# Performance work log

Measured on AMD Instinct MI355X. Metric: run time of the kernel, lower is better.

Reference implementation:

```python
import jax, jax.numpy as jnp
import numpy as np

N, E, L, F, HID, OUT = 20000, 200000, 5, 4, 128, 3


def _lin(x, w, b):
    # torch Linear convention: w is [out, in]
    return x @ w.T + b


def setup_inputs() -> dict:
    key = jax.random.key(0)
    ks = iter(jax.random.split(key, 40))
    nrm = lambda shape, s=0.05: jax.random.normal(next(ks), shape, dtype=jnp.float32) * s
    inp = {
        'x': jax.random.normal(next(ks), (N, L, F), dtype=jnp.float32),
        'edge_index': jax.random.randint(next(ks), (2, E), 0, N, dtype=jnp.int64),
        'edge_attr': jax.random.normal(next(ks), (E, F), dtype=jnp.float32),
        'batch': jnp.zeros((N,), dtype=jnp.int64),
        'node_type': jax.random.normal(next(ks), (N, 1), dtype=jnp.float32),
        # PastStateEncoder params
        'emb': nrm((L, F), 1.0),
        'conv_w': nrm((HID, 2 * F, 3)),  # Conv1d(8,128,3) OIW
        'conv_b': nrm((HID,)),
        # FusionLayer Linear(129,128)
        'fuse_w': nrm((HID, HID + 1)), 'fuse_b': nrm((HID,)),
        # gnn1 EdgeModel: Linear(2*128+4,128), Linear(128,128)
        'g1e_w1': nrm((HID, 2 * HID + F)), 'g1e_b1': nrm((HID,)),
        'g1e_w2': nrm((HID, HID)), 'g1e_b2': nrm((HID,)),
        # gnn1 NodeModel: Linear(256,128), Linear(128,128)
        'g1n_w1': nrm((HID, 2 * HID)), 'g1n_b1': nrm((HID,)),
        'g1n_w2': nrm((HID, HID)), 'g1n_b2': nrm((HID,)),
        # gnn2 EdgeModel: Linear(2*128+128,128), Linear(128,128)
        'g2e_w1': nrm((HID, 3 * HID)), 'g2e_b1': nrm((HID,)),
        'g2e_w2': nrm((HID, HID)), 'g2e_b2': nrm((HID,)),
        # gnn2 NodeModel
        'g2n_w1': nrm((HID, 2 * HID)), 'g2n_b1': nrm((HID,)),
        'g2n_w2': nrm((HID, HID)), 'g2n_b2': nrm((HID,)),
        # final_mlp: Linear(128,128), BN(128), Linear(128,3)
        'fm_w1': nrm((HID, HID)), 'fm_b1': nrm((HID,)),
        'bn_g': jnp.ones((HID,), dtype=jnp.float32), 'bn_b': jnp.zeros((HID,), dtype=jnp.float32),
        'fm_w2': nrm((OUT, HID)), 'fm_b2': nrm((OUT,)),
    }
    return inp


def _encoder(x, emb, conv_w, conv_b):
    # x: [N, L, F]; append learned positional embedding -> [N, L, 2F]
    n = x.shape[0]
    xe = jnp.concatenate([x, jnp.broadcast_to(emb[None], (n, L, F))], axis=-1)
    xc = xe.transpose(0, 2, 1)  # [N, 2F, L]
    y = jax.lax.conv_general_dilated(
        xc, conv_w, window_strides=(1,), padding=[(1, 1)],
        dimension_numbers=('NCW', 'OIW', 'NCW'))
    y = y + conv_b[None, :, None]
    return y.mean(axis=-1)  # [N, HID]


def _edge_mlp(src, dst, ea, w1, b1, w2, b2):
    h = jax.nn.relu(_lin(jnp.concatenate([src, dst, ea], axis=1), w1, b1))
    return _lin(h, w2, b2)


def _node_mlp(x_row, ea, w1, b1, w2, b2):
    h = jax.nn.relu(_lin(jnp.concatenate([x_row, ea], axis=1), w1, b1))
    return _lin(h, w2, b2)


def reference(x, edge_index, edge_attr, batch, node_type,
              emb, conv_w, conv_b, fuse_w, fuse_b,
              g1e_w1, g1e_b1, g1e_w2, g1e_b2, g1n_w1, g1n_b1, g1n_w2, g1n_b2,
              g2e_w1, g2e_b1, g2e_w2, g2e_b2, g2n_w1, g2n_b1, g2n_w2, g2n_b2,
              fm_w1, fm_b1, bn_g, bn_b, fm_w2, fm_b2):
    row, col = edge_index[0], edge_index[1]
    h = _encoder(x, emb, conv_w, conv_b)                     # [N,128]
    h = _lin(jnp.concatenate([h, node_type], axis=-1), fuse_w, fuse_b)  # [N,128]
    # gnn1 (MetaLayer: edge model then node model; node model here is per-edge)
    ea = _edge_mlp(h[row], h[col], edge_attr, g1e_w1, g1e_b1, g1e_w2, g1e_b2)  # [E,128]
    h = _node_mlp(h[row], ea, g1n_w1, g1n_b1, g1n_w2, g1n_b2)                  # [E,128]
    # gnn2 (h now lives on edges; indices < N <= E remain valid, matching torch)
    ea = _edge_mlp(h[row], h[col], ea, g2e_w1, g2e_b1, g2e_w2, g2e_b2)
    h = _node_mlp(h[row], ea, g2n_w1, g2n_b1, g2n_w2, g2n_b2)
    # final head on edge_attr: Linear -> BatchNorm1d (training stats) -> ReLU -> Linear
    z = _lin(ea, fm_w1, fm_b1)
    mu = z.mean(axis=0)
    var = z.var(axis=0)  # biased, matches torch BN normalization
    z = (z - mu) * jax.lax.rsqrt(var + 1e-5) * bn_g + bn_b
    z = jax.nn.relu(z)
    return _lin(z, fm_w2, fm_b2)  # [E,3]
```

## Files before the change

### kernel.cpp

```cpp
#include <hip/hip_runtime.h>

#define N_NODES 20000
#define N_EDGES 200000
#define HID 128
#define STR 136
#define NBLK 3125
#define NREP 64

typedef unsigned short u16;
using bf16x8 = __attribute__((ext_vector_type(8))) __bf16;
using f32x4  = __attribute__((ext_vector_type(4))) float;

__device__ __forceinline__ u16 f2bf(float f) {
  union { float f; unsigned u; } v; v.f = f;
  unsigned u = v.u;
  return (u16)((u + 0x7FFFu + ((u >> 16) & 1u)) >> 16);
}
__device__ __forceinline__ float bf2f(unsigned s) {
  union { unsigned u; float f; } v; v.u = s << 16;
  return v.f;
}
__device__ __forceinline__ bf16x8 ld8(const u16* p) { return *(const bf16x8*)p; }

__device__ __forceinline__ void zero_acc(f32x4 acc[4][2]) {
#pragma unroll
  for (int i = 0; i < 4; ++i) {
    acc[i][0] = (f32x4){0.f, 0.f, 0.f, 0.f};
    acc[i][1] = (f32x4){0.f, 0.f, 0.f, 0.f};
  }
}

template <int KSTEPS, typename AF>
__device__ __forceinline__ void wgemm(const u16* __restrict__ PW, AF afrag,
                                      f32x4 acc[4][2], int lane, int wave) {
  const u16* pb = PW + (wave * 2 * 64 + lane) * 8;
  bf16x8 b0[2], b1[2];
  b0[0] = ld8(pb);
  b1[0] = ld8(pb + 512);
#pragma unroll
  for (int ks = 0; ks < KSTEPS; ++ks) {
    const int cur = ks & 1, nxt = cur ^ 1;
    if (ks + 1 < KSTEPS) {
      b0[nxt] = ld8(pb + (ks + 1) * 4096);
      b1[nxt] = ld8(pb + (ks + 1) * 4096 + 512);
    }
#pragma unroll
    for (int mt = 0; mt < 4; ++mt) {
      bf16x8 a = afrag(ks, mt);
      acc[mt][0] = __builtin_amdgcn_mfma_f32_16x16x32_bf16(a, b0[cur], acc[mt][0], 0, 0, 0);
      acc[mt][1] = __builtin_amdgcn_mfma_f32_16x16x32_bf16(a, b1[cur], acc[mt][1], 0, 0, 0);
    }
  }
}

template <bool RELU>
__device__ __forceinline__ void epi_store(u16* buf, const f32x4 acc[4][2],
                                          const float* __restrict__ bias,
                                          int lane, int wave) {
  const int c = lane & 15, q = lane >> 4;
  const float bb0 = bias[wave * 32 + c], bb1 = bias[wave * 32 + 16 + c];
#pragma unroll
  for (int mt = 0; mt < 4; ++mt)
#pragma unroll
    for (int nt = 0; nt < 2; ++nt) {
      const float bb = nt ? bb1 : bb0;
      const int col = wave * 32 + nt * 16 + c;
#pragma unroll
      for (int r = 0; r < 4; ++r) {
        float v = acc[mt][nt][r] + bb;
        if (RELU) v = fmaxf(v, 0.f);
        buf[(mt * 16 + q * 4 + r) * STR + col] = f2bf(v);
      }
    }
}

__device__ __forceinline__ void flush_buf(const u16* buf, u16* __restrict__ gout,
                                          int e0, int tid) {
#pragma unroll
  for (int it = 0; it < 4; ++it) {
    int cid = tid + it * 256, e = cid >> 4, p = cid & 15;
    uint4 v = *(const uint4*)(buf + e * STR + p * 8);
    *(uint4*)(gout + (size_t)(e0 + e) * HID + p * 8) = v;
  }
}

__device__ __forceinline__ void stage_gather(const int* __restrict__ rowI,
                                             const int* __restrict__ colI,
                                             const u16* __restrict__ htab,
                                             u16* B0, u16* B1,
                                             int e0, int lane, int wave) {
  const int r = lane >> 4, p = lane & 15;
#pragma unroll
  for (int it = 0; it < 8; ++it) {
    int j = wave * 32 + it * 4 + r;
    int e = j & 63;
    int id = (j < 64) ? rowI[e0 + e] : colI[e0 + e];
    uint4 v = *(const uint4*)(htab + (size_t)id * HID + p * 8);
    *(uint4*)(((j < 64) ? B0 : B1) + e * STR + p * 8) = v;
  }
}

__global__ __launch_bounds__(128) void k_prep1(
    const float* __restrict__ emb, const float* __restrict__ conv_w,
    const float* __restrict__ conv_b, const float* __restrict__ fuse_w,
    const float* __restrict__ fuse_b,
    const float* __restrict__ fm_w1, const float* __restrict__ g2e_b2,
    const float* __restrict__ fm_b1, const float* __restrict__ w6,
    float* __restrict__ Mt, float* __restrict__ C0, float* __restrict__ Wnt,
    float* __restrict__ b67, float* __restrict__ W67) {
  __shared__ float red[22][129];
  __shared__ float w7s[128];
  const int o = blockIdx.x;
  const int j = threadIdx.x;
  float A[21];
  {
    float b0 = conv_b[j];
#pragma unroll
    for (int p = 0; p < 5; ++p) {
#pragma unroll
      for (int i = 0; i < 8; ++i) {
        float s = 0.f;
#pragma unroll
        for (int k = 0; k < 3; ++k) {
          int t = p + 1 - k;
          if (t >= 0 && t < 5) s += conv_w[(j * 8 + i) * 3 + k];
        }
        s *= 0.2f;
        if (i < 4) A[p * 4 + i] = s;
        else b0 += emb[p * 4 + (i - 4)] * s;
      }
    }
    A[20] = b0;
  }
  float w = fuse_w[o * 129 + j];
  float w7 = fm_w1[o * 128 + j];
  w7s[j] = w7;
#pragma unroll
  for (int qq = 0; qq < 21; ++qq) red[qq][j] = w * A[qq];
  red[21][j] = w7 * g2e_b2[j];
  __syncthreads();
  if (j < 22) {
    float s = 0.f;
    for (int t = 0; t < 128; ++t) s += red[j][t];
    if (j < 20)      Mt[j * 128 + o] = s;
    else if (j == 20) C0[o] = s + fuse_b[o];
    else              b67[o] = s + fm_b1[o];
  }
  if (j == 0) Wnt[o] = fuse_w[o * 129 + 128];
  float s = 0.f;
  for (int t = 0; t < 128; ++t) s += w7s[t] * w6[t * 128 + j];
  W67[o * 128 + j] = s;
}

struct PackArgs {
  const float* src[6];
  u16* dst[6];
  int Kin[6];
  int ksCum[7];
};

__global__ __launch_bounds__(256) void k_prep2(
    PackArgs pa, const float* __restrict__ x, const float* __restrict__ node_type,
    const float* __restrict__ Mt, const float* __restrict__ C0,
    const float* __restrict__ Wnt, u16* __restrict__ h2) {
  if (blockIdx.x < 41) {
    int bk = blockIdx.x;
    int mi = 0;
    while (bk >= pa.ksCum[mi + 1]) ++mi;
    int ks = bk - pa.ksCum[mi];
    const float* W = pa.src[mi];
    u16* D = pa.dst[mi] + ks * 4096;
    int Kin = pa.Kin[mi];
#pragma unroll
    for (int t = 0; t < 16; ++t) {
      int el = t * 256 + (int)threadIdx.x;
      int j = el & 7, ln = (el >> 3) & 63, ntile = el >> 9;
      int k = ks * 32 + ((ln >> 4) << 3) + j;
      int n = ntile * 16 + (ln & 15);
      float v = (k < Kin) ? W[n * Kin + k] : 0.0f;
      D[el] = f2bf(v);
    }
    return;
  }
  __shared__ float xs[16][20], nts[16], mts[20 * 128];
  const int tid = threadIdx.x;
  const int n0 = ((int)blockIdx.x - 41) * 16;
  for (int i = tid; i < 320; i += 256) xs[i / 20][i % 20] = x[n0 * 20 + i];
  if (tid < 16) nts[tid] = node_type[n0 + tid];
  for (int i = tid; i < 2560; i += 256) mts[i] = Mt[i];
  __syncthreads();
  const int nl = tid >> 4;
  const int c0 = (tid & 15) * 8;
  float nt = nts[nl];
  union { u16 s[8]; uint4 u; } o;
#pragma unroll
  for (int i = 0; i < 8; ++i) {
    int ch = c0 + i;
    float acc = C0[ch] + Wnt[ch] * nt;
#pragma unroll
    for (int qq = 0; qq < 20; ++qq) acc += xs[nl][qq] * mts[qq * 128 + ch];
    o.s[i] = f2bf(acc);
  }
  *(uint4*)(h2 + (size_t)(n0 + nl) * HID + c0) = o.u;
}

__global__ __launch_bounds__(256, 4) void k_gnn1(
    const int* __restrict__ eidx, const float* __restrict__ eattr,
    const u16* __restrict__ h2, const u16* __restrict__ pW1, const u16* __restrict__ pW2,
    const u16* __restrict__ pW3, const u16* __restrict__ pW4, const float* __restrict__ b1,
    const float* __restrict__ b2, const float* __restrict__ b3, const float* __restrict__ b4,
    u16* __restrict__ ea1, u16* __restrict__ h3) {
  __shared__ __align__(16) u16 B0[64 * STR], B1[64 * STR];
  const int tid = threadIdx.x, lane = tid & 63, wave = tid >> 6;
  const int e0 = blockIdx.x * 64;
  const int m = lane & 15, q = lane >> 4;
  const int aoff = m * STR + q * 8;
  const int* rowI = eidx;
  const int* colI = eidx + N_EDGES;

  stage_gather(rowI, colI, h2, B0, B1, e0, lane, wave);

  bf16x8 ef[4];
#pragma unroll
  for (int mt = 0; mt < 4; ++mt) {
    union { u16 s[8]; uint4 u; bf16x8 v; } t;
    t.u = make_uint4(0u, 0u, 0u, 0u);
    if (q == 0) {
      float4 a = *(const float4*)(eattr + (size_t)(e0 + mt * 16 + m) * 4);
      t.s[0] = f2bf(a.x); t.s[1] = f2bf(a.y); t.s[2] = f2bf(a.z); t.s[3] = f2bf(a.w);
    }
    ef[mt] = t.v;
  }
  __syncthreads();

  f32x4 acc[4][2];
  zero_acc(acc);
  wgemm<9>(pW1, [&](int ks, int mt) -> bf16x8 {
    if (ks < 4) return ld8(B0 + aoff + mt * 16 * STR + ks * 32);
    if (ks < 8) return ld8(B1 + aoff + mt * 16 * STR + (ks - 4) * 32);
    return ef[mt];
  }, acc, lane, wave);
  __syncthreads();
  epi_store<true>(B1, acc, b1, lane, wave);
  __syncthreads();

  zero_acc(acc);
  wgemm<4>(pW2, [&](int ks, int mt) -> bf16x8 {
    return ld8(B1 + aoff + mt * 16 * STR + ks * 32);
  }, acc, lane, wave);
  epi_store<false>(B0, acc, b2, lane, wave);
  __syncthreads();
  flush_buf(B0, ea1, e0, tid);

  if (e0 < N_NODES) {
#pragma unroll
    for (int it = 0; it < 4; ++it) {
      int e = wave * 16 + it * 4 + q;
      int id = rowI[e0 + e];
      uint4 v = *(const uint4*)(h2 + (size_t)id * HID + m * 8);
      *(uint4*)(B1 + e * STR + m * 8) = v;
    }
    __syncthreads();

    zero_acc(acc);
    wgemm<8>(pW3, [&](int ks, int mt) -> bf16x8 {
      if (ks < 4) return ld8(B1 + aoff + mt * 16 * STR + ks * 32);
      return ld8(B0 + aoff + mt * 16 * STR + (ks - 4) * 32);
    }, acc, lane, wave);
    __syncthreads();
    epi_store<true>(B1, acc, b3, lane, wave);
    __syncthreads();

    zero_acc(acc);
    wgemm<4>(pW4, [&](int ks, int mt) -> bf16x8 {
      return ld8(B1 + aoff + mt * 16 * STR + ks * 32);
    }, acc, lane, wave);
    epi_store<false>(B0, acc, b4, lane, wave);
    __syncthreads();
    flush_buf(B0, h3, e0, tid);
  }
}

__global__ __launch_bounds__(256, 4) void k_gnn2(
    const int* __restrict__ eidx, const u16* __restrict__ h3, u16* ea1z,
    const u16* __restrict__ pW5, const u16* __restrict__ pW67,
    const float* __restrict__ b5, const float* __restrict__ b67,
    float* __restrict__ bnrep) {
  __shared__ __align__(16) u16 B0[64 * STR], B1[64 * STR];
  const int tid = threadIdx.x, lane = tid & 63, wave = tid >> 6;
  const int e0 = blockIdx.x * 64;
  const int m = lane & 15, q = lane >> 4;
  const int aoff = m * STR + q * 8;
  const int* rowI = eidx;
  const int* colI = eidx + N_EDGES;

  stage_gather(rowI, colI, h3, B0, B1, e0, lane, wave);
  __syncthreads();

  f32x4 acc[4][2];
  zero_acc(acc);
  wgemm<8>(pW5, [&](int ks, int mt) -> bf16x8 {
    if (ks < 4) return ld8(B0 + aoff + mt * 16 * STR + ks * 32);
    return ld8(B1 + aoff + mt * 16 * STR + (ks - 4) * 32);
  }, acc, lane, wave);
  __syncthreads();

#pragma unroll
  for (int it = 0; it < 4; ++it) {
    int cid = tid + it * 256, e = cid >> 4, p = cid & 15;
    uint4 v = *(const uint4*)(ea1z + (size_t)(e0 + e) * HID + p * 8);
    *(uint4*)(B0 + e * STR + p * 8) = v;
  }
  __syncthreads();

  wgemm<4>(pW5 + 8 * 4096, [&](int ks, int mt) -> bf16x8 {
    return ld8(B0 + aoff + mt * 16 * STR + ks * 32);
  }, acc, lane, wave);
  epi_store<true>(B1, acc, b5, lane, wave);
  __syncthreads();

  zero_acc(acc);
  wgemm<4>(pW67, [&](int ks, int mt) -> bf16x8 {
    return ld8(B1 + aoff + mt * 16 * STR + ks * 32);
  }, acc, lane, wave);

  {
    const int c = lane & 15;
    const float bb0 = b67[wave * 32 + c], bb1 = b67[wave * 32 + 16 + c];
    float s0 = 0.f, q0 = 0.f, s1 = 0.f, q1 = 0.f;
#pragma unroll
    for (int mt = 0; mt < 4; ++mt)
#pragma unroll
      for (int r = 0; r < 4; ++r) {
        float v0 = acc[mt][0][r] + bb0;
        float v1 = acc[mt][1][r] + bb1;
        s0 += v0; q0 += v0 * v0;
        s1 += v1; q1 += v1 * v1;
        int row = mt * 16 + q * 4 + r;
        B0[row * STR + wave * 32 + c] = f2bf(v0);
        B0[row * STR + wave * 32 + 16 + c] = f2bf(v1);
      }
    s0 += __shfl_xor(s0, 16); s0 += __shfl_xor(s0, 32);
    q0 += __shfl_xor(q0, 16); q0 += __shfl_xor(q0, 32);
    s1 += __shfl_xor(s1, 16); s1 += __shfl_xor(s1, 32);
    q1 += __shfl_xor(q1, 16); q1 += __shfl_xor(q1, 32);
    if (lane < 16) {
      float* slot = bnrep + ((int)blockIdx.x & (NREP - 1)) * 256;
      atomicAdd(&slot[wave * 32 + lane], s0);
      atomicAdd(&slot[wave * 32 + 16 + lane], s1);
      atomicAdd(&slot[128 + wave * 32 + lane], q0);
      atomicAdd(&slot[128 + wave * 32 + 16 + lane], q1);
    }
  }
  __syncthreads();
  flush_buf(B0, ea1z, e0, tid);
}

__global__ __launch_bounds__(256) void k_head(const u16* __restrict__ z,
                                              const float* __restrict__ bnrep,
                                              const float* __restrict__ bn_g,
                                              const float* __restrict__ bn_b,
                                              const float* __restrict__ w2,
                                              const float* __restrict__ b2,
                                              float* __restrict__ out) {
  __shared__ float sh_s[128], sh_h[128], sh_w0[128], sh_w1[128], sh_w2[128];
  const int tid = threadIdx.x;
  {
    float s = 0.f;
    for (int r = 0; r < NREP; ++r) s += bnrep[r * 256 + tid];
    __shared__ float acc2[256];
    acc2[tid] = s;
    __syncthreads();
    if (tid < 128) {
      const float inv = 1.0f / (float)N_EDGES;
      float mu = acc2[tid] * inv;
      float var = acc2[128 + tid] * inv - mu * mu;
      float sc = bn_g[tid] * rsqrtf(var + 1e-5f);
      sh_s[tid] = sc;
      sh_h[tid] = bn_b[tid] - mu * sc;
      sh_w0[tid] = w2[tid];
      sh_w1[tid] = w2[128 + tid];
      sh_w2[tid] = w2[256 + tid];
    }
    __syncthreads();
  }
  const int lane = tid & 63, wave = tid >> 6;
  const int g = lane >> 4;
  const int p = lane & 15;
  const int c0 = p * 8;
  const float bb0 = b2[0], bb1 = b2[1], bb2 = b2[2];
#pragma unroll 4
  for (int it = 0; it < 16; ++it) {
    int e = (int)blockIdx.x * 256 + wave * 64 + it * 4 + g;
    if (e >= N_EDGES) break;
    uint4 v = *(const uint4*)(z + (size_t)e * HID + c0);
    unsigned wv[4] = {v.x, v.y, v.z, v.w};
    float a0 = 0.f, a1 = 0.f, a2 = 0.f;
#pragma unroll
    for (int k = 0; k < 4; ++k) {
      int ch = c0 + k * 2;
      float lo = bf2f(wv[k] & 0xffffu), hi = bf2f(wv[k] >> 16);
      float r0 = fmaxf(fmaf(lo, sh_s[ch], sh_h[ch]), 0.f);
      float r1 = fmaxf(fmaf(hi, sh_s[ch + 1], sh_h[ch + 1]), 0.f);
      a0 += r0 * sh_w0[ch] + r1 * sh_w0[ch + 1];
      a1 += r0 * sh_w1[ch] + r1 * sh_w1[ch + 1];
      a2 += r0 * sh_w2[ch] + r1 * sh_w2[ch + 1];
    }
#pragma unroll
    for (int off = 1; off < 16; off <<= 1) {
      a0 += __shfl_xor(a0, off);
      a1 += __shfl_xor(a1, off);
      a2 += __shfl_xor(a2, off);
    }
    if (p < 3) out[e * 3 + p] = (p == 0) ? a0 + bb0 : (p == 1) ? a1 + bb1 : a2 + bb2;
  }
}

extern "C" void kernel_launch(void* const* d_in, const int* in_sizes, int n_in,
                              void* d_out, int out_size, void* d_ws, size_t ws_size,
                              hipStream_t stream) {
  const float* x         = (const float*)d_in[0];
  const int* eidx        = (const int*)d_in[1];
  const float* eattr     = (const float*)d_in[2];
  const float* node_type = (const float*)d_in[4];
  const float* emb       = (const float*)d_in[5];
  const float* conv_w    = (const float*)d_in[6];
  const float* conv_b    = (const float*)d_in[7];
  const float* fuse_w    = (const float*)d_in[8];
  const float* fuse_b    = (const float*)d_in[9];
  const float* g1e_w1    = (const float*)d_in[10];
  const float* g1e_b1    = (const float*)d_in[11];
  const float* g1e_w2    = (const float*)d_in[12];
  const float* g1e_b2    = (const float*)d_in[13];
  const float* g1n_w1    = (const float*)d_in[14];
  const float* g1n_b1    = (const float*)d_in[15];
  const float* g1n_w2    = (const float*)d_in[16];
  const float* g1n_b2    = (const float*)d_in[17];
  const float* g2e_w1    = (const float*)d_in[18];
  const float* g2e_b1    = (const float*)d_in[19];
  const float* g2e_w2    = (const float*)d_in[20];
  const float* g2e_b2    = (const float*)d_in[21];
  const float* fm_w1     = (const float*)d_in[26];
  const float* fm_b1     = (const float*)d_in[27];
  const float* bn_g      = (const float*)d_in[28];
  const float* bn_b      = (const float*)d_in[29];
  const float* fm_w2     = (const float*)d_in[30];
  const float* fm_b2     = (const float*)d_in[31];
  float* out = (float*)d_out;

  char* ws = (char*)d_ws;
  size_t off = 0;
  auto take = [&](size_t bytes) {
    void* p = ws + off;
    off = (off + bytes + 255) & ~(size_t)255;
    return p;
  };
  u16* h2   = (u16*)take((size_t)N_NODES * HID * 2);
  u16* h3   = (u16*)take((size_t)20032 * HID * 2);
  u16* ea1z = (u16*)take((size_t)N_EDGES * HID * 2);
  float* Mt    = (float*)take(20 * 128 * 4);
  float* C0    = (float*)take(128 * 4);
  float* Wnt   = (float*)take(128 * 4);
  float* b67   = (float*)take(128 * 4);
  float* W67f  = (float*)take(128 * 128 * 4);
  float* bnrep = (float*)take((size_t)NREP * 256 * 4);
  u16* pW1  = (u16*)take(9 * 4096 * 2);
  u16* pW2  = (u16*)take(4 * 4096 * 2);
  u16* pW3  = (u16*)take(8 * 4096 * 2);
  u16* pW4  = (u16*)take(4 * 4096 * 2);
  u16* pW5  = (u16*)take(12 * 4096 * 2);
  u16* pW67 = (u16*)take(4 * 4096 * 2);

  hipMemsetAsync(bnrep, 0, (size_t)NREP * 256 * 4, stream);
  k_prep1<<<128, 128, 0, stream>>>(emb, conv_w, conv_b, fuse_w, fuse_b,
                                   fm_w1, g2e_b2, fm_b1, g2e_w2,
                                   Mt, C0, Wnt, b67, W67f);

  PackArgs pa;
  const float* srcs[6] = {g1e_w1, g1e_w2, g1n_w1, g1n_w2, g2e_w1, W67f};
  u16* dsts[6] = {pW1, pW2, pW3, pW4, pW5, pW67};
  int kins[6] = {260, 128, 256, 128, 384, 128};
  int kst[6] = {9, 4, 8, 4, 12, 4};
  int cum = 0;
  for (int i = 0; i < 6; ++i) {
    pa.src[i] = srcs[i]; pa.dst[i] = dsts[i]; pa.Kin[i] = kins[i];
    pa.ksCum[i] = cum; cum += kst[i];
  }
  pa.ksCum[6] = cum;

  k_prep2<<<41 + N_NODES / 16, 256, 0, stream>>>(pa, x, node_type, Mt, C0, Wnt, h2);
  k_gnn1<<<NBLK, 256, 0, stream>>>(eidx, eattr, h2, pW1, pW2, pW3, pW4,
                                   g1e_b1, g1e_b2, g1n_b1, g1n_b2, ea1z, h3);
  k_gnn2<<<NBLK, 256, 0, stream>>>(eidx, h3, ea1z, pW5, pW67,
                                   g2e_b1, b67, bnrep);
  k_head<<<(N_EDGES + 255) / 256, 256, 0, stream>>>(ea1z, bnrep, bn_g, bn_b,
                                                    fm_w2, fm_b2, out);
}
```

Baseline: 236.8 us.

## Split GNN edge tiles across eight waves and fold BN-stat zeroing into prep

The two GNN kernels move from 4 waves per 64-edge block, each computing 32 output columns, to 8 waves per block, each computing 16 columns. Per-thread accumulators and B-fragment prefetch are halved, and the gather and flush loops are rebalanced over 512 threads. The aim is more resident waves per CU and lower register pressure so gather latency is better hidden. In exchange each wave does less MFMA work per A-fragment load from LDS, so LDS traffic rises. Separately, the hipMemsetAsync of the BN statistics buffer is replaced by zeroing it inside k_prep1, which drops one launch.

Result: no change. 232.4 us (median of 2 runs) (-1.9%).

```diff
diff --git a/kernel.cpp b/kernel.cpp
--- a/kernel.cpp
+++ b/kernel.cpp
@@ -22,77 +22,65 @@
 }
 __device__ __forceinline__ bf16x8 ld8(const u16* p) { return *(const bf16x8*)p; }
 
-__device__ __forceinline__ void zero_acc(f32x4 acc[4][2]) {
-#pragma unroll
-  for (int i = 0; i < 4; ++i) {
-    acc[i][0] = (f32x4){0.f, 0.f, 0.f, 0.f};
-    acc[i][1] = (f32x4){0.f, 0.f, 0.f, 0.f};
-  }
+__device__ __forceinline__ void zero_acc8(f32x4 acc[4]) {
+#pragma unroll
+  for (int i = 0; i < 4; ++i) acc[i] = (f32x4){0.f, 0.f, 0.f, 0.f};
 }
 
 template <int KSTEPS, typename AF>
-__device__ __forceinline__ void wgemm(const u16* __restrict__ PW, AF afrag,
-                                      f32x4 acc[4][2], int lane, int wave) {
-  const u16* pb = PW + (wave * 2 * 64 + lane) * 8;
-  bf16x8 b0[2], b1[2];
-  b0[0] = ld8(pb);
-  b1[0] = ld8(pb + 512);
+__device__ __forceinline__ void wgemm8(const u16* __restrict__ PW, AF afrag,
+                                       f32x4 acc[4], int lane, int wave) {
+  const u16* pb = PW + (wave * 64 + lane) * 8;
+  bf16x8 b[2];
+  b[0] = ld8(pb);
 #pragma unroll
   for (int ks = 0; ks < KSTEPS; ++ks) {
-    const int cur = ks & 1, nxt = cur ^ 1;
-    if (ks + 1 < KSTEPS) {
-      b0[nxt] = ld8(pb + (ks + 1) * 4096);
-      b1[nxt] = ld8(pb + (ks + 1) * 4096 + 512);
-    }
+    const int cur = ks & 1;
+    if (ks + 1 < KSTEPS) b[cur ^ 1] = ld8(pb + (ks + 1) * 4096);
 #pragma unroll
     for (int mt = 0; mt < 4; ++mt) {
       bf16x8 a = afrag(ks, mt);
-      acc[mt][0] = __builtin_amdgcn_mfma_f32_16x16x32_bf16(a, b0[cur], acc[mt][0], 0, 0, 0);
-      acc[mt][1] = __builtin_amdgcn_mfma_f32_16x16x32_bf16(a, b1[cur], acc[mt][1], 0, 0, 0);
+      acc[mt] = __builtin_amdgcn_mfma_f32_16x16x32_bf16(a, b[cur], acc[mt], 0, 0, 0);
     }
   }
 }
 
 template <bool RELU>
-__device__ __forceinline__ void epi_store(u16* buf, const f32x4 acc[4][2],
-                                          const float* __restrict__ bias,
-                                          int lane, int wave) {
+__device__ __forceinline__ void epi_store8(u16* buf, const f32x4 acc[4],
+                                           const float* __restrict__ bias,
+                                           int lane, int wave) {
   const int c = lane & 15, q = lane >> 4;
-  const float bb0 = bias[wave * 32 + c], bb1 = bias[wave * 32 + 16 + c];
+  const float bb = bias[wave * 16 + c];
+  const int col = wave * 16 + c;
 #pragma unroll
   for (int mt = 0; mt < 4; ++mt)
 #pragma unroll
-    for (int nt = 0; nt < 2; ++nt) {
-      const float bb = nt ? bb1 : bb0;
-      const int col = wave * 32 + nt * 16 + c;
-#pragma unroll
-      for (int r = 0; r < 4; ++r) {
-        float v = acc[mt][nt][r] + bb;
-        if (RELU) v = fmaxf(v, 0.f);
-        buf[(mt * 16 + q * 4 + r) * STR + col] = f2bf(v);
-      }
-    }
-}
-
-__device__ __forceinline__ void flush_buf(const u16* buf, u16* __restrict__ gout,
-                                          int e0, int tid) {
-#pragma unroll
-  for (int it = 0; it < 4; ++it) {
-    int cid = tid + it * 256, e = cid >> 4, p = cid & 15;
+    for (int r = 0; r < 4; ++r) {
+      float v = acc[mt][r] + bb;
+      if (RELU) v = fmaxf(v, 0.f);
+      buf[(mt * 16 + q * 4 + r) * STR + col] = f2bf(v);
+    }
+}
+
+__device__ __forceinline__ void flush_buf8(const u16* buf, u16* __restrict__ gout,
+                                           int e0, int tid) {
+#pragma unroll
+  for (int it = 0; it < 2; ++it) {
+    int cid = tid + it * 512, e = cid >> 4, p = cid & 15;
     uint4 v = *(const uint4*)(buf + e * STR + p * 8);
     *(uint4*)(gout + (size_t)(e0 + e) * HID + p * 8) = v;
   }
 }
 
-__device__ __forceinline__ void stage_gather(const int* __restrict__ rowI,
-                                             const int* __restrict__ colI,
-                                             const u16* __restrict__ htab,
-                                             u16* B0, u16* B1,
-                                             int e0, int lane, int wave) {
+__device__ __forceinline__ void stage_gather8(const int* __restrict__ rowI,
+                                              const int* __restrict__ colI,
+                                              const u16* __restrict__ htab,
+                                              u16* B0, u16* B1,
+                                              int e0, int lane, int wave) {
   const int r = lane >> 4, p = lane & 15;
 #pragma unroll
-  for (int it = 0; it < 8; ++it) {
-    int j = wave * 32 + it * 4 + r;
+  for (int it = 0; it < 4; ++it) {
+    int j = wave * 16 + it * 4 + r;
     int e = j & 63;
     int id = (j < 64) ? rowI[e0 + e] : colI[e0 + e];
     uint4 v = *(const uint4*)(htab + (size_t)id * HID + p * 8);
@@ -107,11 +95,12 @@
     const float* __restrict__ fm_w1, const float* __restrict__ g2e_b2,
     const float* __restrict__ fm_b1, const float* __restrict__ w6,
     float* __restrict__ Mt, float* __restrict__ C0, float* __restrict__ Wnt,
-    float* __restrict__ b67, float* __restrict__ W67) {
+    float* __restrict__ b67, float* __restrict__ W67, float* __restrict__ bnrep) {
   __shared__ float red[22][129];
   __shared__ float w7s[128];
   const int o = blockIdx.x;
   const int j = threadIdx.x;
+  bnrep[o * 128 + j] = 0.f;
   float A[21];
   {
     float b0 = conv_b[j];
@@ -204,7 +193,7 @@
   *(uint4*)(h2 + (size_t)(n0 + nl) * HID + c0) = o.u;
 }
 
-__global__ __launch_bounds__(256, 4) void k_gnn1(
+__global__ __launch_bounds__(512, 8) void k_gnn1(
     const int* __restrict__ eidx, const float* __restrict__ eattr,
     const u16* __restrict__ h2, const u16* __restrict__ pW1, const u16* __restrict__ pW2,
     const u16* __restrict__ pW3, const u16* __restrict__ pW4, const float* __restrict__ b1,
@@ -218,7 +207,7 @@
   const int* rowI = eidx;
   const int* colI = eidx + N_EDGES;
 
-  stage_gather(rowI, colI, h2, B0, B1, e0, lane, wave);
+  stage_gather8(rowI, colI, h2, B0, B1, e0, lane, wave);
 
   bf16x8 ef[4];
 #pragma unroll
@@ -233,55 +222,55 @@
   }
   __syncthreads();
 
-  f32x4 acc[4][2];
-  zero_acc(acc);
-  wgemm<9>(pW1, [&](int ks, int mt) -> bf16x8 {
+  f32x4 acc[4];
+  zero_acc8(acc);
+  wgemm8<9>(pW1, [&](int ks, int mt) -> bf16x8 {
     if (ks < 4) return ld8(B0 + aoff + mt * 16 * STR + ks * 32);
     if (ks < 8) return ld8(B1 + aoff + mt * 16 * STR + (ks - 4) * 32);
     return ef[mt];
   }, acc, lane, wave);
   __syncthreads();
-  epi_store<true>(B1, acc, b1, lane, wave);
-  __syncthreads();
-
-  zero_acc(acc);
-  wgemm<4>(pW2, [&](int ks, int mt) -> bf16x8 {
+  epi_store8<true>(B1, acc, b1, lane, wave);
+  __syncthreads();
+
+  zero_acc8(acc);
+  wgemm8<4>(pW2, [&](int ks, int mt) -> bf16x8 {
     return ld8(B1 + aoff + mt * 16 * STR + ks * 32);
   }, acc, lane, wave);
-  epi_store<false>(B0, acc, b2, lane, wave);
-  __syncthreads();
-  flush_buf(B0, ea1, e0, tid);
+  epi_store8<false>(B0, acc, b2, lane, wave);
+  __syncthreads();
+  flush_buf8(B0, ea1, e0, tid);
 
   if (e0 < N_NODES) {
 #pragma unroll
-    for (int it = 0; it < 4; ++it) {
-      int e = wave * 16 + it * 4 + q;
+    for (int it = 0; it < 2; ++it) {
+      int e = wave * 8 + it * 4 + q;
       int id = rowI[e0 + e];
       uint4 v = *(const uint4*)(h2 + (size_t)id * HID + m * 8);
       *(uint4*)(B1 + e * STR + m * 8) = v;
     }
     __syncthreads();
 
-    zero_acc(acc);
-    wgemm<8>(pW3, [&](int ks, int mt) -> bf16x8 {
+    zero_acc8(acc);
+    wgemm8<8>(pW3, [&](int ks, int mt) -> bf16x8 {
       if (ks < 4) return ld8(B1 + aoff + mt * 16 * STR + ks * 32);
       return ld8(B0 + aoff + mt * 16 * STR + (ks - 4) * 32);
     }, acc, lane, wave);
     __syncthreads();
-    epi_store<true>(B1, acc, b3, lane, wave);
-    __syncthreads();
-
-    zero_acc(acc);
-    wgemm<4>(pW4, [&](int ks, int mt) -> bf16x8 {
+    epi_store8<true>(B1, acc, b3, lane, wave);
+    __syncthreads();
+
+    zero_acc8(acc);
+    wgemm8<4>(pW4, [&](int ks, int mt) -> bf16x8 {
       return ld8(B1 + aoff + mt * 16 * STR + ks * 32);
     }, acc, lane, wave);
-    epi_store<false>(B0, acc, b4, lane, wave);
-    __syncthreads();
-    flush_buf(B0, h3, e0, tid);
-  }
-}
-
-__global__ __launch_bounds__(256, 4) void k_gnn2(
+    epi_store8<false>(B0, acc, b4, lane, wave);
+    __syncthreads();
+    flush_buf8(B0, h3, e0, tid);
+  }
+}
+
+__global__ __launch_bounds__(512, 8) void k_gnn2(
     const int* __restrict__ eidx, const u16* __restrict__ h3, u16* ea1z,
     const u16* __restrict__ pW5, const u16* __restrict__ pW67,
     const float* __restrict__ b5, const float* __restrict__ b67,
@@ -294,66 +283,60 @@
   const int* rowI = eidx;
   const int* colI = eidx + N_EDGES;
 
-  stage_gather(rowI, colI, h3, B0, B1, e0, lane, wave);
-  __syncthreads();
-
-  f32x4 acc[4][2];
-  zero_acc(acc);
-  wgemm<8>(pW5, [&](int ks, int mt) -> bf16x8 {
+  stage_gather8(rowI, colI, h3, B0, B1, e0, lane, wave);
+  __syncthreads();
+
+  f32x4 acc[4];
+  zero_acc8(acc);
+  wgemm8<8>(pW5, [&](int ks, int mt) -> bf16x8 {
     if (ks < 4) return ld8(B0 + aoff + mt * 16 * STR + ks * 32);
     return ld8(B1 + aoff + mt * 16 * STR + (ks - 4) * 32);
   }, acc, lane, wave);
   __syncthreads();
 
 #pragma unroll
-  for (int it = 0; it < 4; ++it) {
-    int cid = tid + it * 256, e = cid >> 4, p = cid & 15;
+  for (int it = 0; it < 2; ++it) {
+    int cid = tid + it * 512, e = cid >> 4, p = cid & 15;
     uint4 v = *(const uint4*)(ea1z + (size_t)(e0 + e) * HID + p * 8);
     *(uint4*)(B0 + e * STR + p * 8) = v;
   }
   __syncthreads();
 
-  wgemm<4>(pW5 + 8 * 4096, [&](int ks, int mt) -> bf16x8 {
+  wgemm8<4>(pW5 + 8 * 4096, [&](int ks, int mt) -> bf16x8 {
     return ld8(B0 + aoff + mt * 16 * STR + ks * 32);
   }, acc, lane, wave);
-  epi_store<true>(B1, acc, b5, lane, wave);
-  __syncthreads();
-
-  zero_acc(acc);
-  wgemm<4>(pW67, [&](int ks, int mt) -> bf16x8 {
+  epi_store8<true>(B1, acc, b5, lane, wave);
+  __syncthreads();
+
+  zero_acc8(acc);
+  wgemm8<4>(pW67, [&](int ks, int mt) -> bf16x8 {
     return ld8(B1 + aoff + mt * 16 * STR + ks * 32);
   }, acc, lane, wave);
 
   {
     const int c = lane & 15;
-    const float bb0 = b67[wave * 32 + c], bb1 = b67[wave * 32 + 16 + c];
-    float s0 = 0.f, q0 = 0.f, s1 = 0.f, q1 = 0.f;
+    const int col = wave * 16 + c;
+    const float bb = b67[col];
+    float s0 = 0.f, q0 = 0.f;
 #pragma unroll
     for (int mt = 0; mt < 4; ++mt)
 #pragma unroll
       for (int r = 0; r < 4; ++r) {
-        float v0 = acc[mt][0][r] + bb0;
-        float v1 = acc[mt][1][r] + bb1;
+        float v0 = acc[mt][r] + bb;
         s0 += v0; q0 += v0 * v0;
-        s1 += v1; q1 += v1 * v1;
         int row = mt * 16 + q * 4 + r;
-        B0[row * STR + wave * 32 + c] = f2bf(v0);
-        B0[row * STR + wave * 32 + 16 + c] = f2bf(v1);
+        B0[row * STR + col] = f2bf(v0);
       }
     s0 += __shfl_xor(s0, 16); s0 += __shfl_xor(s0, 32);
     q0 += __shfl_xor(q0, 16); q0 += __shfl_xor(q0, 32);
-    s1 += __shfl_xor(s1, 16); s1 += __shfl_xor(s1, 32);
-    q1 += __shfl_xor(q1, 16); q1 += __shfl_xor(q1, 32);
     if (lane < 16) {
       float* slot = bnrep + ((int)blockIdx.x & (NREP - 1)) * 256;
-      atomicAdd(&slot[wave * 32 + lane], s0);
-      atomicAdd(&slot[wave * 32 + 16 + lane], s1);
-      atomicAdd(&slot[128 + wave * 32 + lane], q0);
-      atomicAdd(&slot[128 + wave * 32 + 16 + lane], q1);
-    }
-  }
-  __syncthreads();
-  flush_buf(B0, ea1z, e0, tid);
+      atomicAdd(&slot[wave * 16 + lane], s0);
+      atomicAdd(&slot[128 + wave * 16 + lane], q0);
+    }
+  }
+  __syncthreads();
+  flush_buf8(B0, ea1z, e0, tid);
 }
 
 __global__ __launch_bounds__(256) void k_head(const u16* __restrict__ z,
@@ -471,10 +454,9 @@
   u16* pW5  = (u16*)take(12 * 4096 * 2);
   u16* pW67 = (u16*)take(4 * 4096 * 2);
 
-  hipMemsetAsync(bnrep, 0, (size_t)NREP * 256 * 4, stream);
   k_prep1<<<128, 128, 0, stream>>>(emb, conv_w, conv_b, fuse_w, fuse_b,
                                    fm_w1, g2e_b2, fm_b1, g2e_w2,
-                                   Mt, C0, Wnt, b67, W67f);
+                                   Mt, C0, Wnt, b67, W67f, bnrep);
 
   PackArgs pa;
   const float* srcs[6] = {g1e_w1, g1e_w2, g1n_w1, g1n_w2, g2e_w1, W67f};
@@ -489,9 +471,9 @@
   pa.ksCum[6] = cum;
 
   k_prep2<<<41 + N_NODES / 16, 256, 0, stream>>>(pa, x, node_type, Mt, C0, Wnt, h2);
-  k_gnn1<<<NBLK, 256, 0, stream>>>(eidx, eattr, h2, pW1, pW2, pW3, pW4,
+  k_gnn1<<<NBLK, 512, 0, stream>>>(eidx, eattr, h2, pW1, pW2, pW3, pW4,
                                    g1e_b1, g1e_b2, g1n_b1, g1n_b2, ea1z, h3);
-  k_gnn2<<<NBLK, 256, 0, stream>>>(eidx, h3, ea1z, pW5, pW67,
+  k_gnn2<<<NBLK, 512, 0, stream>>>(eidx, h3, ea1z, pW5, pW67,
                                    g2e_b1, b67, bnrep);
   k_head<<<(N_EDGES + 255) / 256, 256, 0, stream>>>(ea1z, bnrep, bn_g, bn_b,
                                                     fm_w2, fm_b2, out);
```
